# Kernel optimization log

Measured on AMD Instinct MI355X. Metric: run time of the kernel, lower is better.

## Reference

```python
import jax, jax.numpy as jnp
import numpy as np

B, L, D, H, K = 4, 4096, 1024, 16, 256

def setup_inputs() -> dict:
    key = jax.random.key(0)
    ks = jax.random.split(key, 11)
    s = 0.02
    return {
        "x": jax.random.normal(ks[0], (B, L, D), jnp.float32),
        "Wq": jax.random.normal(ks[1], (D, D), jnp.float32) * s,
        "bq": jax.random.normal(ks[2], (D,), jnp.float32) * s,
        "Wk": jax.random.normal(ks[3], (D, D), jnp.float32) * s,
        "bk": jax.random.normal(ks[4], (D,), jnp.float32) * s,
        "Wv": jax.random.normal(ks[5], (D, D), jnp.float32) * s,
        "bv": jax.random.normal(ks[6], (D,), jnp.float32) * s,
        "E": jax.random.normal(ks[7], (L, K), jnp.float32),
        "F": jax.random.normal(ks[8], (L, K), jnp.float32),
        "Wo": jax.random.normal(ks[9], (D, D), jnp.float32) * s,
        "bo": jax.random.normal(ks[10], (D,), jnp.float32) * s,
        "n_heads": H,
    }

def reference(x, Wq, bq, Wk, bk, Wv, bv, E, F, Wo, bo, n_heads):
    Bc, Lc, Dc = x.shape
    hd = Dc // n_heads
    scale = hd ** -0.5
    # QKV projections (torch Linear: x @ W.T + b; here W stored as [in,out])
    q = (x @ Wq + bq).reshape(Bc, Lc, n_heads, hd)  # blhd
    k = (x @ Wk + bk).reshape(Bc, Lc, n_heads, hd)
    v = (x @ Wv + bv).reshape(Bc, Lc, n_heads, hd)
    # Low-rank projection of K/V sequence dim: L -> K
    kE = jnp.einsum('blhd,lk->bhkd', k, E[:Lc])
    vF = jnp.einsum('blhd,lk->bhkd', v, F[:Lc])
    # Attention over compressed dim k
    qk = jnp.einsum('blhd,bhkd->bhlk', q, kE) * scale
    attn = jax.nn.softmax(qk, axis=-1)
    out = jnp.einsum('bhlk,bhkd->blhd', attn, vF).reshape(Bc, Lc, Dc)
    return out @ Wo + bo
```

## Files before the change

### kernel.cpp

```cpp
#include <hip/hip_runtime.h>

typedef _Float16 half_t;
typedef __attribute__((ext_vector_type(8))) _Float16 f16x8;
typedef __attribute__((ext_vector_type(4))) _Float16 f16x4;
typedef __attribute__((ext_vector_type(4))) float f32x4;
typedef __attribute__((ext_vector_type(4))) float float4v;

__device__ __forceinline__ void gload_lds16(const void* g, void* l) {
  __builtin_amdgcn_global_load_lds(
      (const __attribute__((address_space(1))) void*)g,
      (__attribute__((address_space(3))) void*)l, 16, 0, 0);
}

template<int OUTF16>
__global__ __launch_bounds__(512, 2)
void gemm_big(const half_t* __restrict__ A, const half_t* __restrict__ Bt,
              void* __restrict__ Cv, const float* __restrict__ bias, float alpha)
{
  __shared__ __attribute__((aligned(16))) char lds[131072];
  const int tid = threadIdx.x, w = tid >> 6, lane = tid & 63;
  const int wr = w >> 2, wc = w & 3;
  const int g = lane >> 4, cc = lane & 15;
  const int m0 = blockIdx.x * 256, n0 = blockIdx.y * 256;

  const int srow2 = tid >> 2, sslot = tid & 3;
  const int swslot = sslot ^ ((srow2 >> 1) & 3);
  const int swr = (g ^ ((cc >> 1) & 3)) << 4;

  const f32x4 zero = {0.f, 0.f, 0.f, 0.f};
  f32x4 acc[8][4];
#pragma unroll
  for (int i = 0; i < 8; ++i)
#pragma unroll
    for (int j = 0; j < 4; ++j) acc[i][j] = zero;

  auto STAGE_HALF = [&](int ktile, int hh, char* sb) {
    const int kk = hh >> 1, isB = hh & 1;
    const half_t* src = isB ? Bt : A;
    const int base_row = isB ? n0 : m0;
    const long rowoff = (long)(base_row + srow2) * 1024 + ktile * 64 + kk * 32 + swslot * 8;
    char* d = sb + isB * 32768 + kk * 16384;
    gload_lds16(src + rowoff,          d + tid * 16);
    gload_lds16(src + rowoff + 131072, d + 8192 + tid * 16);
  };

  {
    char* b0 = lds;
    STAGE_HALF(0, 0, b0); STAGE_HALF(0, 1, b0);
    STAGE_HALF(0, 2, b0); STAGE_HALF(0, 3, b0);
  }
  asm volatile("s_waitcnt vmcnt(4)" ::: "memory");
  __builtin_amdgcn_s_barrier();

#pragma unroll 1
  for (int n = 0; n < 16; ++n) {
    const char* rb = lds + ((n & 1) << 16);
    char* sb = lds + (((n + 1) & 1) << 16);
    f16x8 bf[4];
#pragma unroll
    for (int ph = 0; ph < 4; ++ph) {
      const int kk = ph >> 1, fh = ph & 1;
      f16x8 af[4];
      const char* Ah = rb + kk * 16384;
#pragma unroll
      for (int mf = 0; mf < 4; ++mf)
        af[mf] = *(const f16x8*)(Ah + (wr * 128 + fh * 64 + mf * 16 + cc) * 64 + swr);
      if (fh == 0) {
        const char* Bh = rb + 32768 + kk * 16384;
#pragma unroll
        for (int nf = 0; nf < 4; ++nf)
          bf[nf] = *(const f16x8*)(Bh + (wc * 64 + nf * 16 + cc) * 64 + swr);
      }
      if (n < 15) STAGE_HALF(n + 1, ph, sb);
      __builtin_amdgcn_sched_barrier(0);
      __builtin_amdgcn_s_barrier();
      asm volatile("s_waitcnt lgkmcnt(0)" ::: "memory");
      __builtin_amdgcn_sched_barrier(0);
      __builtin_amdgcn_s_setprio(1);
#pragma unroll
      for (int mf = 0; mf < 4; ++mf)
#pragma unroll
        for (int nf = 0; nf < 4; ++nf)
          acc[fh * 4 + mf][nf] =
              __builtin_amdgcn_mfma_f32_16x16x32_f16(af[mf], bf[nf], acc[fh * 4 + mf][nf], 0, 0, 0);
      __builtin_amdgcn_s_setprio(0);
      __builtin_amdgcn_sched_barrier(0);
      if (ph == 1) {
        if (n < 15) { asm volatile("s_waitcnt vmcnt(4)" ::: "memory"); }
        else        { asm volatile("s_waitcnt vmcnt(0)" ::: "memory"); }
      } else if (ph == 3) {
        if (n < 15) { asm volatile("s_waitcnt vmcnt(4)" ::: "memory"); }
      }
      __builtin_amdgcn_s_barrier();
    }
  }

#pragma unroll
  for (int mf = 0; mf < 8; ++mf)
#pragma unroll
    for (int nf = 0; nf < 4; ++nf)
#pragma unroll
      for (int r = 0; r < 4; ++r) {
        const int row = m0 + wr * 128 + mf * 16 + g * 4 + r;
        const int col = n0 + wc * 64 + nf * 16 + cc;
        float v = (acc[mf][nf][r] + bias[col]) * alpha;
        if (OUTF16) ((half_t*)Cv)[(long)row * 1024 + col] = (half_t)v;
        else        ((float*)Cv)[(long)row * 1024 + col] = v;
      }
}

template<int BM, int BN, int WM, int WN, int OUTF16, int MODE, int SK>
__global__ __launch_bounds__(256, 2)
void gemm_bt(const half_t* __restrict__ A, const half_t* __restrict__ Bt,
             void* __restrict__ Cv, const float* __restrict__ bias,
             const float* __restrict__ rowscale,
             int M, int N, int K, int lda, int ldb, int ldc, float alpha,
             long sA, long sB, long sC)
{
  constexpr int FM = WM / 16, FN = WN / 16, CW = BN / WN;
  __shared__ __attribute__((aligned(16))) half_t As[BM * 32];
  __shared__ __attribute__((aligned(16))) half_t Bs[BN * 32];

  const int tid = threadIdx.x, w = tid >> 6, lane = tid & 63;
  const int wr = w / CW, wc = w % CW;
  const int z = blockIdx.z / SK, ks = blockIdx.z % SK;
  const half_t* Ab = A + (long)z * sA;
  const half_t* Bb = Bt + (long)z * sB;
  const int m0 = blockIdx.x * BM, n0 = blockIdx.y * BN;
  const int g = lane >> 4, cc = lane & 15;
  const int srow = lane >> 2, scol = (lane & 3) * 8;

  const f32x4 zero = {0.f, 0.f, 0.f, 0.f};
  f32x4 acc[FM][FN];
#pragma unroll
  for (int i = 0; i < FM; ++i)
#pragma unroll
    for (int j = 0; j < FN; ++j) acc[i][j] = zero;

  const int kchunk = K / SK;
  for (int kt = ks * kchunk; kt < (ks + 1) * kchunk; kt += 32) {
#pragma unroll
    for (int j = 0; j < BM / 64; ++j) {
      const int bi = w * (BM / 64) + j;
      gload_lds16(Ab + (long)(m0 + bi * 16 + srow) * lda + kt + scol, &As[bi * 512]);
    }
#pragma unroll
    for (int j = 0; j < BN / 64; ++j) {
      const int bi = w * (BN / 64) + j;
      gload_lds16(Bb + (long)(n0 + bi * 16 + srow) * ldb + kt + scol, &Bs[bi * 512]);
    }
    __syncthreads();

    f16x8 af[FM], bf[FN];
#pragma unroll
    for (int i = 0; i < FM; ++i)
      af[i] = *(const f16x8*)&As[(wr * WM + i * 16 + cc) * 32 + g * 8];
#pragma unroll
    for (int j = 0; j < FN; ++j)
      bf[j] = *(const f16x8*)&Bs[(wc * WN + j * 16 + cc) * 32 + g * 8];
#pragma unroll
    for (int i = 0; i < FM; ++i)
#pragma unroll
      for (int j = 0; j < FN; ++j)
        acc[i][j] = __builtin_amdgcn_mfma_f32_16x16x32_f16(af[i], bf[j], acc[i][j], 0, 0, 0);
    __syncthreads();
  }

  const long coff = (long)z * sC;
#pragma unroll
  for (int i = 0; i < FM; ++i)
#pragma unroll
    for (int j = 0; j < FN; ++j)
#pragma unroll
      for (int r = 0; r < 4; ++r) {
        const int row = m0 + wr * WM + i * 16 + g * 4 + r;
        const int col = n0 + wc * WN + j * 16 + cc;
        float v = acc[i][j][r];
        if (MODE == 1) v = (v + bias[col]) * alpha;
        if (MODE == 2 || MODE == 4) v = v + rowscale[row] * bias[col];
        if (MODE == 3) {
          const int nb = gridDim.z / SK;
          ((float*)Cv)[((long)ks * nb + z) * sC + (long)row * ldc + col] = v;
        } else if (MODE == 4) {
          ((half_t*)Cv)[coff + (long)(col >> 6) * ((long)M * 64) + (long)row * 64 + (col & 63)]
              = (half_t)v;
        } else {
          if (OUTF16) ((half_t*)Cv)[coff + (long)row * ldc + col] = (half_t)v;
          else        ((float*)Cv)[coff + (long)row * ldc + col] = v;
        }
      }
}

__global__ __launch_bounds__(512, 2)
void attn_fused(const half_t* __restrict__ q, const half_t* __restrict__ kEh,
                const half_t* __restrict__ vFt, half_t* __restrict__ outp, int L)
{
  __shared__ __attribute__((aligned(16))) half_t Ks[256 * 64];
  __shared__ __attribute__((aligned(16))) half_t Vs[64 * 256];
  const int tid = threadIdx.x, w = tid >> 6, lane = tid & 63;
  const int g = lane >> 4, c = lane & 15;
  const int l0 = blockIdx.x * 256, h = blockIdx.y, b = blockIdx.z;

  const half_t* keh = kEh + (long)(b * 16 + h) * 16384;
  const half_t* vfh = vFt + (long)b * 262144 + (long)h * 16384;
  const half_t* qb  = q + ((long)b * L + l0 + w * 32) * 1024 + h * 64;
  half_t* ob = outp + ((long)b * L + l0 + w * 32) * 1024 + h * 64;

#pragma unroll
  for (int i = 0; i < 4; ++i) {
    const int row = i * 64 + (tid >> 3), slot = tid & 7;
    gload_lds16(keh + row * 64 + ((slot ^ (row & 7)) << 3),
                (char*)Ks + i * 8192 + tid * 16);
  }
#pragma unroll
  for (int i = 0; i < 4; ++i) {
    const int row = i * 16 + (tid >> 5), slot = tid & 31;
    gload_lds16(vfh + row * 256 + ((slot ^ (row & 7)) << 3),
                (char*)Vs + i * 8192 + tid * 16);
  }

  f16x8 qf[2][2];
#pragma unroll
  for (int fi = 0; fi < 2; ++fi)
#pragma unroll
    for (int ks = 0; ks < 2; ++ks)
      qf[fi][ks] = *(const f16x8*)(qb + (long)(fi * 16 + c) * 1024 + ks * 32 + g * 8);

  __syncthreads();

  const f32x4 zero = {0.f, 0.f, 0.f, 0.f};
  f32x4 o[2][4];
#pragma unroll
  for (int fi = 0; fi < 2; ++fi)
#pragma unroll
    for (int fd = 0; fd < 4; ++fd) o[fi][fd] = zero;
  float mrun[2] = {-3.0e38f, -3.0e38f};
  float lrun[2] = {0.f, 0.f};

  for (int ch = 0; ch < 4; ++ch) {
    f32x4 s[2][4];
#pragma unroll
    for (int fi = 0; fi < 2; ++fi)
#pragma unroll
      for (int fj = 0; fj < 4; ++fj) s[fi][fj] = zero;
#pragma unroll
    for (int fj = 0; fj < 4; ++fj) {
      const int krow = ch * 64 + fj * 16 + c;
      const char* kb = (const char*)Ks + krow * 128;
      f16x8 k0 = *(const f16x8*)(kb + ((g ^ (c & 7)) << 4));
      f16x8 k1 = *(const f16x8*)(kb + (((4 + g) ^ (c & 7)) << 4));
#pragma unroll
      for (int fi = 0; fi < 2; ++fi) {
        s[fi][fj] = __builtin_amdgcn_mfma_f32_16x16x32_f16(k0, qf[fi][0], s[fi][fj], 0, 0, 0);
        s[fi][fj] = __builtin_amdgcn_mfma_f32_16x16x32_f16(k1, qf[fi][1], s[fi][fj], 0, 0, 0);
      }
    }

    f16x4 p[2][4];
#pragma unroll
    for (int fi = 0; fi < 2; ++fi) {
      float cm = -3.0e38f;
#pragma unroll
      for (int fj = 0; fj < 4; ++fj)
#pragma unroll
        for (int r = 0; r < 4; ++r) cm = fmaxf(cm, s[fi][fj][r]);
      cm = fmaxf(cm, __shfl_xor(cm, 16));
      cm = fmaxf(cm, __shfl_xor(cm, 32));
      const float mnew = fmaxf(mrun[fi], cm);
      const float sc = __expf(mrun[fi] - mnew);
      float csum = 0.f;
#pragma unroll
      for (int fj = 0; fj < 4; ++fj) {
        f16x4 fr;
#pragma unroll
        for (int r = 0; r < 4; ++r) {
          float e = __expf(s[fi][fj][r] - mnew);
          fr[r] = (half_t)e; csum += e;
        }
        p[fi][fj] = fr;
      }
      csum += __shfl_xor(csum, 16);
      csum += __shfl_xor(csum, 32);
      lrun[fi] = lrun[fi] * sc + csum;
      mrun[fi] = mnew;
#pragma unroll
      for (int fd = 0; fd < 4; ++fd)
#pragma unroll
        for (int r = 0; r < 4; ++r) o[fi][fd][r] *= sc;
    }

#pragma unroll
    for (int kc = 0; kc < 4; ++kc) {
      const int s16 = ch * 8 + kc * 2 + (g >> 1);
      f16x4 va[4];
#pragma unroll
      for (int fd = 0; fd < 4; ++fd) {
        const int drow = fd * 16 + c;
        va[fd] = *(const f16x4*)((const char*)Vs + drow * 512 +
                                 ((s16 ^ (c & 7)) << 4) + (g & 1) * 8);
      }
#pragma unroll
      for (int fi = 0; fi < 2; ++fi)
#pragma unroll
        for (int fd = 0; fd < 4; ++fd)
          o[fi][fd] = __builtin_amdgcn_mfma_f32_16x16x16f16(va[fd], p[fi][kc], o[fi][fd], 0, 0, 0);
    }
  }

#pragma unroll
  for (int fi = 0; fi < 2; ++fi) {
    const float inv = 1.0f / lrun[fi];
#pragma unroll
    for (int fd = 0; fd < 4; ++fd) {
      f16x4 st;
#pragma unroll
      for (int r = 0; r < 4; ++r) st[r] = (half_t)(o[fi][fd][r] * inv);
      *(f16x4*)(ob + (long)(fi * 16 + c) * 1024 + fd * 16 + g * 4) = st;
    }
  }
}

__global__ void reduce4_f16(const float* __restrict__ in, half_t* __restrict__ out) {
  long i = ((long)blockIdx.x * 256 + threadIdx.x) * 4;
  float4v a = *(const float4v*)(in + i);
#pragma unroll
  for (int ks = 1; ks < 4; ++ks) {
    float4v t = *(const float4v*)(in + (long)ks * 2097152 + i);
    a.x += t.x; a.y += t.y; a.z += t.z; a.w += t.w;
  }
  f16x4 o;
  o[0] = (half_t)a.x; o[1] = (half_t)a.y; o[2] = (half_t)a.z; o[3] = (half_t)a.w;
  *(f16x4*)(out + i) = o;
}

__global__ void xpass(const float* __restrict__ x, half_t* __restrict__ xhf,
                      half_t* __restrict__ xT) {
  __shared__ float t[32][33];
  const int b = blockIdx.z, d0 = blockIdx.x * 32, l0 = blockIdx.y * 32;
  const int tx = threadIdx.x, ty = threadIdx.y;
  const float* ip = x + ((long)b * 4096 + l0) * 1024 + d0;
  half_t* oh = xhf + ((long)b * 4096 + l0) * 1024 + d0;
#pragma unroll
  for (int j = 0; j < 4; ++j) {
    float v = ip[(long)(ty + 8 * j) * 1024 + tx];
    t[ty + 8 * j][tx] = v;
    oh[(long)(ty + 8 * j) * 1024 + tx] = (half_t)v;
  }
  __syncthreads();
  half_t* ot = xT + ((long)b * 1024 + d0) * 4096 + l0;
#pragma unroll
  for (int j = 0; j < 4; ++j)
    ot[(long)(ty + 8 * j) * 4096 + tx] = (half_t)t[tx][ty + 8 * j];
}

__global__ void efpass(const float* __restrict__ in, half_t* __restrict__ outT,
                       float* __restrict__ ssum) {
  __shared__ float t[32][33];
  __shared__ float ps[8][32];
  const int k0 = blockIdx.x * 32, l0 = blockIdx.y * 32;
  const int tx = threadIdx.x, ty = threadIdx.y;
  float p = 0.f;
#pragma unroll
  for (int j = 0; j < 4; ++j) {
    float v = in[(long)(l0 + ty + 8 * j) * 256 + k0 + tx];
    t[ty + 8 * j][tx] = v; p += v;
  }
  ps[ty][tx] = p;
  __syncthreads();
  if (ty == 0) {
    float a = 0.f;
#pragma unroll
    for (int r = 0; r < 8; ++r) a += ps[r][tx];
    atomicAdd(&ssum[k0 + tx], a);
  }
#pragma unroll
  for (int j = 0; j < 4; ++j)
    outT[(long)(k0 + ty + 8 * j) * 4096 + l0 + tx] = (half_t)t[tx][ty + 8 * j];
}

__global__ void transpose_f32_f16(const float* __restrict__ in, half_t* __restrict__ out,
                                  int R, int C) {
  __shared__ float t[32][33];
  const int cx = blockIdx.x * 32 + threadIdx.x;
  const int r0 = blockIdx.y * 32;
#pragma unroll
  for (int j = 0; j < 4; ++j)
    t[threadIdx.y + 8 * j][threadIdx.x] = in[(long)(r0 + threadIdx.y + 8 * j) * C + cx];
  __syncthreads();
  const int rx = r0 + threadIdx.x;
  const int cy = blockIdx.x * 32 + threadIdx.y;
#pragma unroll
  for (int j = 0; j < 4; ++j)
    out[(long)(cy + 8 * j) * R + rx] = (half_t)t[threadIdx.x][threadIdx.y + 8 * j];
}

extern "C" void kernel_launch(void* const* d_in, const int* in_sizes, int n_in,
                              void* d_out, int out_size, void* d_ws, size_t ws_size,
                              hipStream_t stream)
{
  const float* x  = (const float*)d_in[0];
  const float* Wq = (const float*)d_in[1];
  const float* bq = (const float*)d_in[2];
  const float* Wk = (const float*)d_in[3];
  const float* bk = (const float*)d_in[4];
  const float* Wv = (const float*)d_in[5];
  const float* bv = (const float*)d_in[6];
  const float* E  = (const float*)d_in[7];
  const float* F  = (const float*)d_in[8];
  const float* Wo = (const float*)d_in[9];
  const float* bo = (const float*)d_in[10];
  float* out = (float*)d_out;

  char* ws = (char*)d_ws;
  half_t* xhf  = (half_t*)(ws);
  half_t* xT   = (half_t*)(ws + 33554432);
  half_t* qhf  = (half_t*)(ws + 67108864);
  half_t* Wqt  = (half_t*)(ws + 100663296);
  half_t* Wkt  = Wqt + 1048576;
  half_t* Wvt  = Wkt + 1048576;
  half_t* Wot  = Wvt + 1048576;
  half_t* EFt  = (half_t*)(ws + 109051904);
  half_t* xEF  = (half_t*)(ws + 113246208);
  half_t* kEb  = (half_t*)(ws + 117440512);
  half_t* vFtb = (half_t*)(ws + 119537664);
  float*  sEF  = (float*)(ws + 121634816);
  half_t* outp = xhf;
  float*  xEFf = (float*)d_out;

  hipMemsetAsync(sEF, 0, 2048, stream);
  dim3 tb(32, 8);
  xpass<<<dim3(32, 128, 4), tb, 0, stream>>>(x, xhf, xT);
  efpass<<<dim3(8, 128, 1), tb, 0, stream>>>(E, EFt, sEF);
  efpass<<<dim3(8, 128, 1), tb, 0, stream>>>(F, EFt + 1048576, sEF + 256);
  transpose_f32_f16<<<dim3(32, 32, 1), tb, 0, stream>>>(Wq, Wqt, 1024, 1024);
  transpose_f32_f16<<<dim3(32, 32, 1), tb, 0, stream>>>(Wk, Wkt, 1024, 1024);
  transpose_f32_f16<<<dim3(32, 32, 1), tb, 0, stream>>>(Wv, Wvt, 1024, 1024);
  transpose_f32_f16<<<dim3(32, 32, 1), tb, 0, stream>>>(Wo, Wot, 1024, 1024);

  gemm_bt<128,128,64,64,0,3,4><<<dim3(4, 8, 16), 256, 0, stream>>>(
      EFt, xT, (void*)xEFf, nullptr, nullptr, 512, 1024, 4096, 4096, 4096, 1024, 1.f,
      0, 4194304, 524288);
  reduce4_f16<<<2048, 256, 0, stream>>>(xEFf, xEF);

  gemm_big<1><<<dim3(64, 4), 512, 0, stream>>>(xhf, Wqt, qhf, bq, 0.125f);
  gemm_bt<128,128,64,64,1,4,1><<<dim3(2, 8, 4), 256, 0, stream>>>(
      xEF, Wkt, kEb, bk, sEF, 256, 1024, 1024, 1024, 1024, 1024, 1.f,
      524288, 0, 262144);
  gemm_bt<128,128,64,64,1,2,1><<<dim3(8, 2, 4), 256, 0, stream>>>(
      Wvt, xEF + 262144, vFtb, sEF + 256, bv, 1024, 256, 1024, 1024, 1024, 256, 1.f,
      0, 524288, 262144);
  attn_fused<<<dim3(16, 16, 4), 512, 0, stream>>>(qhf, kEb, vFtb, outp, 4096);
  gemm_big<0><<<dim3(64, 4), 512, 0, stream>>>(outp, Wot, (void*)out, bo, 1.0f);
  (void)in_sizes; (void)n_in; (void)out_size; (void)ws_size;
}
```

Before: 250.5 us.

## Store Q head-major, stage Q via LDS, merge prep launches, shrink small GEMM tiles

The Q projection GEMM now writes its output in a per-head [b,h,l,64] layout. The attention kernel can then load each 256x64 Q panel contiguously into LDS through async global-to-LDS copies, instead of doing strided 1024-stride register loads. The E/F transpose passes and the four weight transposes are each merged into a single launch using blockIdx.z, which cuts launch count. The kE/vF GEMMs switch to 64x64 tiles so they launch more blocks on the small problem. The Q epilogue stores become scattered 2-byte writes, and attention gains an extra LDS round trip and barrier.

```diff
diff --git a/kernel.cpp b/kernel.cpp
--- a/kernel.cpp
+++ b/kernel.cpp
@@ -12,7 +12,7 @@
       (__attribute__((address_space(3))) void*)l, 16, 0, 0);
 }
 
-template<int OUTF16>
+template<int OUTMODE>
 __global__ __launch_bounds__(512, 2)
 void gemm_big(const half_t* __restrict__ A, const half_t* __restrict__ Bt,
               void* __restrict__ Cv, const float* __restrict__ bias, float alpha)
@@ -104,8 +104,14 @@
         const int row = m0 + wr * 128 + mf * 16 + g * 4 + r;
         const int col = n0 + wc * 64 + nf * 16 + cc;
         float v = (acc[mf][nf][r] + bias[col]) * alpha;
-        if (OUTF16) ((half_t*)Cv)[(long)row * 1024 + col] = (half_t)v;
-        else        ((float*)Cv)[(long)row * 1024 + col] = v;
+        if (OUTMODE == 0) {
+          ((float*)Cv)[(long)row * 1024 + col] = v;
+        } else if (OUTMODE == 1) {
+          ((half_t*)Cv)[(long)row * 1024 + col] = (half_t)v;
+        } else {
+          const int bb = row >> 12, l = row & 4095, h = col >> 6, d = col & 63;
+          ((half_t*)Cv)[(((long)(bb * 16 + h) * 4096 + l) << 6) + d] = (half_t)v;
+        }
       }
 }
 
@@ -192,7 +198,7 @@
 }
 
 __global__ __launch_bounds__(512, 2)
-void attn_fused(const half_t* __restrict__ q, const half_t* __restrict__ kEh,
+void attn_fused(const half_t* __restrict__ qhb, const half_t* __restrict__ kEh,
                 const half_t* __restrict__ vFt, half_t* __restrict__ outp, int L)
 {
   __shared__ __attribute__((aligned(16))) half_t Ks[256 * 64];
@@ -203,8 +209,27 @@
 
   const half_t* keh = kEh + (long)(b * 16 + h) * 16384;
   const half_t* vfh = vFt + (long)b * 262144 + (long)h * 16384;
-  const half_t* qb  = q + ((long)b * L + l0 + w * 32) * 1024 + h * 64;
+  const half_t* qpan = qhb + ((long)(b * 16 + h) * 4096 + l0) * 64;
   half_t* ob = outp + ((long)b * L + l0 + w * 32) * 1024 + h * 64;
+
+#pragma unroll
+  for (int i = 0; i < 4; ++i) {
+    const int row = i * 64 + (tid >> 3), slot = tid & 7;
+    gload_lds16(qpan + row * 64 + ((slot ^ (row & 7)) << 3),
+                (char*)Ks + i * 8192 + tid * 16);
+  }
+  __syncthreads();
+
+  f16x8 qf[2][2];
+#pragma unroll
+  for (int fi = 0; fi < 2; ++fi) {
+    const int qrow = w * 32 + fi * 16 + c;
+    const char* qp = (const char*)Ks + qrow * 128;
+#pragma unroll
+    for (int ks = 0; ks < 2; ++ks)
+      qf[fi][ks] = *(const f16x8*)(qp + (((ks * 4 + g) ^ (qrow & 7)) << 4));
+  }
+  __syncthreads();
 
 #pragma unroll
   for (int i = 0; i < 4; ++i) {
@@ -218,14 +243,6 @@
     gload_lds16(vfh + row * 256 + ((slot ^ (row & 7)) << 3),
                 (char*)Vs + i * 8192 + tid * 16);
   }
-
-  f16x8 qf[2][2];
-#pragma unroll
-  for (int fi = 0; fi < 2; ++fi)
-#pragma unroll
-    for (int ks = 0; ks < 2; ++ks)
-      qf[fi][ks] = *(const f16x8*)(qb + (long)(fi * 16 + c) * 1024 + ks * 32 + g * 8);
-
   __syncthreads();
 
   const f32x4 zero = {0.f, 0.f, 0.f, 0.f};
@@ -353,10 +370,14 @@
     ot[(long)(ty + 8 * j) * 4096 + tx] = (half_t)t[tx][ty + 8 * j];
 }
 
-__global__ void efpass(const float* __restrict__ in, half_t* __restrict__ outT,
-                       float* __restrict__ ssum) {
+__global__ void efpass(const float* __restrict__ E, const float* __restrict__ F,
+                       half_t* __restrict__ outT, float* __restrict__ ssum) {
   __shared__ float t[32][33];
   __shared__ float ps[8][32];
+  const int zz = blockIdx.z;
+  const float* in = zz ? F : E;
+  half_t* oT = outT + (long)zz * 1048576;
+  float* sm = ssum + zz * 256;
   const int k0 = blockIdx.x * 32, l0 = blockIdx.y * 32;
   const int tx = threadIdx.x, ty = threadIdx.y;
   float p = 0.f;
@@ -371,27 +392,32 @@
     float a = 0.f;
 #pragma unroll
     for (int r = 0; r < 8; ++r) a += ps[r][tx];
-    atomicAdd(&ssum[k0 + tx], a);
+    atomicAdd(&sm[k0 + tx], a);
   }
 #pragma unroll
   for (int j = 0; j < 4; ++j)
-    outT[(long)(k0 + ty + 8 * j) * 4096 + l0 + tx] = (half_t)t[tx][ty + 8 * j];
-}
-
-__global__ void transpose_f32_f16(const float* __restrict__ in, half_t* __restrict__ out,
-                                  int R, int C) {
+    oT[(long)(k0 + ty + 8 * j) * 4096 + l0 + tx] = (half_t)t[tx][ty + 8 * j];
+}
+
+__global__ void transposeW(const float* __restrict__ W0, const float* __restrict__ W1,
+                           const float* __restrict__ W2, const float* __restrict__ W3,
+                           half_t* __restrict__ out0, half_t* __restrict__ out1,
+                           half_t* __restrict__ out2, half_t* __restrict__ out3) {
   __shared__ float t[32][33];
+  const int zz = blockIdx.z;
+  const float* in = (zz == 0) ? W0 : (zz == 1) ? W1 : (zz == 2) ? W2 : W3;
+  half_t* out = (zz == 0) ? out0 : (zz == 1) ? out1 : (zz == 2) ? out2 : out3;
   const int cx = blockIdx.x * 32 + threadIdx.x;
   const int r0 = blockIdx.y * 32;
 #pragma unroll
   for (int j = 0; j < 4; ++j)
-    t[threadIdx.y + 8 * j][threadIdx.x] = in[(long)(r0 + threadIdx.y + 8 * j) * C + cx];
+    t[threadIdx.y + 8 * j][threadIdx.x] = in[(long)(r0 + threadIdx.y + 8 * j) * 1024 + cx];
   __syncthreads();
   const int rx = r0 + threadIdx.x;
   const int cy = blockIdx.x * 32 + threadIdx.y;
 #pragma unroll
   for (int j = 0; j < 4; ++j)
-    out[(long)(cy + 8 * j) * R + rx] = (half_t)t[threadIdx.x][threadIdx.y + 8 * j];
+    out[(long)(cy + 8 * j) * 1024 + rx] = (half_t)t[threadIdx.x][threadIdx.y + 8 * j];
 }
 
 extern "C" void kernel_launch(void* const* d_in, const int* in_sizes, int n_in,
@@ -430,23 +456,19 @@
   hipMemsetAsync(sEF, 0, 2048, stream);
   dim3 tb(32, 8);
   xpass<<<dim3(32, 128, 4), tb, 0, stream>>>(x, xhf, xT);
-  efpass<<<dim3(8, 128, 1), tb, 0, stream>>>(E, EFt, sEF);
-  efpass<<<dim3(8, 128, 1), tb, 0, stream>>>(F, EFt + 1048576, sEF + 256);
-  transpose_f32_f16<<<dim3(32, 32, 1), tb, 0, stream>>>(Wq, Wqt, 1024, 1024);
-  transpose_f32_f16<<<dim3(32, 32, 1), tb, 0, stream>>>(Wk, Wkt, 1024, 1024);
-  transpose_f32_f16<<<dim3(32, 32, 1), tb, 0, stream>>>(Wv, Wvt, 1024, 1024);
-  transpose_f32_f16<<<dim3(32, 32, 1), tb, 0, stream>>>(Wo, Wot, 1024, 1024);
+  efpass<<<dim3(8, 128, 2), tb, 0, stream>>>(E, F, EFt, sEF);
+  transposeW<<<dim3(32, 32, 4), tb, 0, stream>>>(Wq, Wk, Wv, Wo, Wqt, Wkt, Wvt, Wot);
 
   gemm_bt<128,128,64,64,0,3,4><<<dim3(4, 8, 16), 256, 0, stream>>>(
       EFt, xT, (void*)xEFf, nullptr, nullptr, 512, 1024, 4096, 4096, 4096, 1024, 1.f,
       0, 4194304, 524288);
   reduce4_f16<<<2048, 256, 0, stream>>>(xEFf, xEF);
 
-  gemm_big<1><<<dim3(64, 4), 512, 0, stream>>>(xhf, Wqt, qhf, bq, 0.125f);
-  gemm_bt<128,128,64,64,1,4,1><<<dim3(2, 8, 4), 256, 0, stream>>>(
+  gemm_big<2><<<dim3(64, 4), 512, 0, stream>>>(xhf, Wqt, qhf, bq, 0.125f);
+  gemm_bt<64,64,32,32,1,4,1><<<dim3(4, 16, 4), 256, 0, stream>>>(
       xEF, Wkt, kEb, bk, sEF, 256, 1024, 1024, 1024, 1024, 1024, 1.f,
       524288, 0, 262144);
-  gemm_bt<128,128,64,64,1,2,1><<<dim3(8, 2, 4), 256, 0, stream>>>(
+  gemm_bt<64,64,32,32,1,2,1><<<dim3(16, 4, 4), 256, 0, stream>>>(
       Wvt, xEF + 262144, vFtb, sEF + 256, bv, 1024, 256, 1024, 1024, 1024, 256, 1.f,
       0, 524288, 262144);
   attn_fused<<<dim3(16, 16, 4), 512, 0, stream>>>(qhf, kEb, vFtb, outp, 4096);
```

Measured after the change: 226.5 us. 1.11x faster.
